# Performance work log

Hardware: AMD Instinct MI355X
Metric: run time of the kernel (lower is better)

Reference implementation:

```python
import jax, jax.numpy as jnp
import numpy as np

B, A, H, V, L = 8192, 128, 256, 64, 20


def setup_inputs() -> dict:
    key = jax.random.key(0)
    ks = jax.random.split(key, 9)
    s = lambda k, sh: jax.random.normal(k, sh, dtype=jnp.float32) * 0.05
    return {
        "attrVector": jax.random.normal(ks[0], (B, A), dtype=jnp.float32),
        "W_a": s(ks[1], (H, A)), "b_a": s(ks[2], (H,)),
        "W_ih": s(ks[3], (4 * H, V)), "W_hh": s(ks[4], (4 * H, H)),
        "b_ih": s(ks[5], (4 * H,)), "b_hh": s(ks[6], (4 * H,)),
        "W_v": s(ks[7], (V, H)), "b_v": s(ks[8], (V,)),
    }


def _lstm_step(x, h, c, W_ih, W_hh, b_ih, b_hh):
    # PyTorch LSTM gate order: input, forget, cell(g), output
    gates = x @ W_ih.T + b_ih + h @ W_hh.T + b_hh  # [B, 4H]
    i, f, g, o = jnp.split(gates, 4, axis=-1)
    c_new = jax.nn.sigmoid(f) * c + jax.nn.sigmoid(i) * jnp.tanh(g)
    h_new = jax.nn.sigmoid(o) * jnp.tanh(c_new)
    return h_new, c_new


def reference(attrVector, W_a, b_a, W_ih, W_hh, b_ih, b_hh, W_v, b_v):
    batch = attrVector.shape[0]
    dt = attrVector.dtype
    # attr2hidden -> initial hidden state; cell state zeros (init_hidden)
    h = attrVector @ W_a.T + b_a                      # [B, H]
    c = jnp.zeros_like(h)
    # start-token step (all-zeros embedding)
    x0 = jnp.zeros((batch, V), dtype=dt)
    h, c = _lstm_step(x0, h, c, W_ih, W_hh, b_ih, b_hh)

    keys = jax.random.split(jax.random.key(42), L)

    def step(carry, k):
        h, c, slp, plp, ep = carry
        logits = h @ W_v.T + b_v                      # [B, V]
        logp = jax.nn.log_softmax(logits, axis=-1)
        plp = plp + jnp.sum(jnp.exp(logp) * logp, axis=-1)  # negative entropy
        ch = jax.random.categorical(k, logits, axis=-1)     # [B] int sample
        lp = jnp.take_along_axis(logp, ch[:, None], axis=-1)[:, 0]
        slp = slp + lp
        ep = ep * jnp.exp(lp)
        x = jax.nn.one_hot(ch, V, dtype=dt)
        h2, c2 = _lstm_step(x, h, c, W_ih, W_hh, b_ih, b_hh)
        return (h2, c2, slp, plp, ep), ch

    zeros = jnp.zeros((batch,), dtype=dt)
    ones = jnp.ones((batch,), dtype=dt)
    (_, _, slp, plp, ep), msgs = jax.lax.scan(step, (h, c, zeros, zeros, ones), keys)
    message = msgs.T.astype(jnp.int64) if msgs.dtype != jnp.int64 else msgs.T  # [B, L]
    return message, slp, plp, ep
```

## Files before the change

### kernel.cpp

```cpp
#include <hip/hip_runtime.h>
#include <stdint.h>

#define BATCH 8192
#define ADIM 128
#define HDIM 256
#define VDIM 64
#define NSTEP 20
#define TB 16
#define HSP 20

typedef union { float4 v; float f[4]; } F4;

__device__ __forceinline__ uint32_t rotl32(uint32_t x, uint32_t d) {
  return (x << d) | (x >> (32u - d));
}
__device__ __forceinline__ void tf4(uint32_t& x0, uint32_t& x1, int r0, int r1, int r2, int r3) {
  x0 += x1; x1 = rotl32(x1, r0); x1 ^= x0;
  x0 += x1; x1 = rotl32(x1, r1); x1 ^= x0;
  x0 += x1; x1 = rotl32(x1, r2); x1 ^= x0;
  x0 += x1; x1 = rotl32(x1, r3); x1 ^= x0;
}
__device__ __forceinline__ void threefry2x32(uint32_t k0, uint32_t k1, uint32_t x0, uint32_t x1,
                                             uint32_t& o0, uint32_t& o1) {
  uint32_t k2 = k0 ^ k1 ^ 0x1BD11BDAu;
  x0 += k0; x1 += k1;
  tf4(x0, x1, 13, 15, 26, 6);  x0 += k1; x1 += k2 + 1u;
  tf4(x0, x1, 17, 29, 16, 24); x0 += k2; x1 += k0 + 2u;
  tf4(x0, x1, 13, 15, 26, 6);  x0 += k0; x1 += k1 + 3u;
  tf4(x0, x1, 17, 29, 16, 24); x0 += k1; x1 += k2 + 4u;
  tf4(x0, x1, 13, 15, 26, 6);  x0 += k2; x1 += k0 + 5u;
  o0 = x0; o1 = x1;
}

__device__ __forceinline__ float sigm(float x) { return 1.0f / (1.0f + expf(-x)); }

__global__ void prep_kernel(const float* __restrict__ Whh, const float* __restrict__ Wv,
                            const float* __restrict__ Wa, const float* __restrict__ Wih,
                            float* __restrict__ ws) {
  int n = blockIdx.x * blockDim.x + threadIdx.x;
  int stride = gridDim.x * blockDim.x;
  float* WhhT4 = ws;
  float* WvT   = ws + 262144;
  float* WaT   = ws + 278528;
  float* WihT4 = ws + 311296;
  for (int i = n; i < 256 * 1024; i += stride) {
    int k = i >> 10, rem = i & 1023, u = rem >> 2, g = rem & 3;
    WhhT4[i] = Whh[((g << 8) + u) * 256 + k];
  }
  for (int i = n; i < 256 * 64; i += stride) { int k = i >> 6, v = i & 63; WvT[i] = Wv[v * 256 + k]; }
  for (int i = n; i < 128 * 256; i += stride) { int k = i >> 8, u = i & 255; WaT[i] = Wa[u * 128 + k]; }
  for (int i = n; i < 64 * 1024; i += stride) {
    int v = i >> 10, rem = i & 1023, u = rem >> 2, g = rem & 3;
    WihT4[i] = Wih[((g << 8) + u) * 64 + v];
  }
}

__global__ __launch_bounds__(256, 2) void sender_main(
    const float* __restrict__ attr, const float* __restrict__ b_a,
    const float* __restrict__ b_ih, const float* __restrict__ b_hh,
    const float* __restrict__ b_v,
    const float* __restrict__ WhhT4, const float* __restrict__ WvT,
    const float* __restrict__ WaT, const float* __restrict__ WihT4,
    float* __restrict__ out) {
  __shared__ float h_s[HDIM][HSP];
  __shared__ float attr_s[ADIM][HSP];
  __shared__ float slp_s[TB], plp_s[TB], ep_s[TB];
  __shared__ int ch_s[TB];

  const int tid = threadIdx.x;
  const int w = tid >> 6;
  const int lane = tid & 63;
  const int u = (w << 6) + lane;
  const int w4 = w << 2;
  const int b0 = blockIdx.x * TB;

  if (tid < TB) { slp_s[tid] = 0.0f; plp_s[tid] = 0.0f; ep_s[tid] = 1.0f; }

  {
    int r = tid >> 5;
    int cm = (tid & 31) << 2;
    #pragma unroll
    for (int pass = 0; pass < 2; ++pass) {
      int row = r + (pass << 3);
      F4 vv; vv.v = *(const float4*)&attr[(size_t)(b0 + row) * ADIM + cm];
      attr_s[cm + 0][row] = vv.f[0];
      attr_s[cm + 1][row] = vv.f[1];
      attr_s[cm + 2][row] = vv.f[2];
      attr_s[cm + 3][row] = vv.f[3];
    }
  }
  __syncthreads();

  {
    float acc[16];
    #pragma unroll
    for (int s = 0; s < 16; ++s) acc[s] = 0.0f;
    #pragma unroll 2
    for (int k = 0; k < ADIM; ++k) {
      F4 a0, a1, a2, a3;
      a0.v = *(const float4*)&attr_s[k][0];
      a1.v = *(const float4*)&attr_s[k][4];
      a2.v = *(const float4*)&attr_s[k][8];
      a3.v = *(const float4*)&attr_s[k][12];
      float wa = WaT[(k << 8) + u];
      #pragma unroll
      for (int j = 0; j < 4; ++j) {
        acc[j]      = fmaf(a0.f[j], wa, acc[j]);
        acc[4 + j]  = fmaf(a1.f[j], wa, acc[4 + j]);
        acc[8 + j]  = fmaf(a2.f[j], wa, acc[8 + j]);
        acc[12 + j] = fmaf(a3.f[j], wa, acc[12 + j]);
      }
    }
    float ba = b_a[u];
    #pragma unroll
    for (int q = 0; q < 4; ++q) {
      F4 hv4;
      #pragma unroll
      for (int j = 0; j < 4; ++j) hv4.f[j] = acc[q * 4 + j] + ba;
      *(float4*)&h_s[u][q * 4] = hv4.v;
    }
  }
  __syncthreads();

  float c_r[16];
  #pragma unroll
  for (int s = 0; s < 16; ++s) c_r[s] = 0.0f;

  float bg[4];
  #pragma unroll
  for (int g = 0; g < 4; ++g) bg[g] = b_ih[(g << 8) + u] + b_hh[(g << 8) + u];
  const float bv = b_v[lane];

  {
    float ga[16][4];
    #pragma unroll
    for (int s = 0; s < 16; ++s)
      #pragma unroll
      for (int g = 0; g < 4; ++g) ga[s][g] = 0.0f;
    #pragma unroll 2
    for (int k = 0; k < HDIM; ++k) {
      F4 h0q, h1q, h2q, h3q;
      h0q.v = *(const float4*)&h_s[k][0];
      h1q.v = *(const float4*)&h_s[k][4];
      h2q.v = *(const float4*)&h_s[k][8];
      h3q.v = *(const float4*)&h_s[k][12];
      F4 wv4; wv4.v = *(const float4*)&WhhT4[(k << 10) + (u << 2)];
      #pragma unroll
      for (int j = 0; j < 4; ++j) {
        #pragma unroll
        for (int g = 0; g < 4; ++g) {
          ga[j][g]      = fmaf(h0q.f[j], wv4.f[g], ga[j][g]);
          ga[4 + j][g]  = fmaf(h1q.f[j], wv4.f[g], ga[4 + j][g]);
          ga[8 + j][g]  = fmaf(h2q.f[j], wv4.f[g], ga[8 + j][g]);
          ga[12 + j][g] = fmaf(h3q.f[j], wv4.f[g], ga[12 + j][g]);
        }
      }
    }
    __syncthreads();
    float hn[16];
    #pragma unroll
    for (int s = 0; s < 16; ++s) {
      float gi = ga[s][0] + bg[0];
      float gf = ga[s][1] + bg[1];
      float gg = ga[s][2] + bg[2];
      float go = ga[s][3] + bg[3];
      float cn = sigm(gf) * c_r[s] + sigm(gi) * tanhf(gg);
      hn[s] = sigm(go) * tanhf(cn);
      c_r[s] = cn;
    }
    #pragma unroll
    for (int q = 0; q < 4; ++q) {
      F4 hv4;
      #pragma unroll
      for (int j = 0; j < 4; ++j) hv4.f[j] = hn[q * 4 + j];
      *(float4*)&h_s[u][q * 4] = hv4.v;
    }
    __syncthreads();
  }

  for (int l = 0; l < NSTEP; ++l) {
    uint32_t kl0, kl1;
    threefry2x32(0u, 42u, 0u, (uint32_t)l, kl0, kl1);

    const bool last = (l == NSTEP - 1);
    float la[4] = {0.0f, 0.0f, 0.0f, 0.0f};
    float ga[16][4];
    #pragma unroll
    for (int s = 0; s < 16; ++s)
      #pragma unroll
      for (int g = 0; g < 4; ++g) ga[s][g] = 0.0f;

    if (!last) {
      #pragma unroll 2
      for (int k = 0; k < HDIM; ++k) {
        F4 h0q, h1q, h2q, h3q, hl;
        h0q.v = *(const float4*)&h_s[k][0];
        h1q.v = *(const float4*)&h_s[k][4];
        h2q.v = *(const float4*)&h_s[k][8];
        h3q.v = *(const float4*)&h_s[k][12];
        hl.v  = *(const float4*)&h_s[k][w4];
        F4 wv4; wv4.v = *(const float4*)&WhhT4[(k << 10) + (u << 2)];
        float wvv = WvT[(k << 6) | lane];
        #pragma unroll
        for (int s = 0; s < 4; ++s) la[s] = fmaf(hl.f[s], wvv, la[s]);
        #pragma unroll
        for (int j = 0; j < 4; ++j) {
          #pragma unroll
          for (int g = 0; g < 4; ++g) {
            ga[j][g]      = fmaf(h0q.f[j], wv4.f[g], ga[j][g]);
            ga[4 + j][g]  = fmaf(h1q.f[j], wv4.f[g], ga[4 + j][g]);
            ga[8 + j][g]  = fmaf(h2q.f[j], wv4.f[g], ga[8 + j][g]);
            ga[12 + j][g] = fmaf(h3q.f[j], wv4.f[g], ga[12 + j][g]);
          }
        }
      }
    } else {
      #pragma unroll 2
      for (int k = 0; k < HDIM; ++k) {
        F4 hl; hl.v = *(const float4*)&h_s[k][w4];
        float wvv = WvT[(k << 6) | lane];
        #pragma unroll
        for (int s = 0; s < 4; ++s) la[s] = fmaf(hl.f[s], wvv, la[s]);
      }
    }

    #pragma unroll
    for (int db = 0; db < 4; ++db) {
      float x = la[db] + bv;
      float m = x;
      #pragma unroll
      for (int o = 32; o > 0; o >>= 1) m = fmaxf(m, __shfl_xor(m, o));
      float e = expf(x - m);
      float s = e;
      #pragma unroll
      for (int o = 32; o > 0; o >>= 1) s += __shfl_xor(s, o);
      float lse = logf(s);
      float logp = x - m - lse;
      float p = expf(logp);
      float pe = p * logp;
      #pragma unroll
      for (int o = 32; o > 0; o >>= 1) pe += __shfl_xor(pe, o);
      uint32_t idx = ((uint32_t)(b0 + w4 + db) << 6) | (uint32_t)lane;
      uint32_t r0, r1;
      threefry2x32(kl0, kl1, 0u, idx, r0, r1);
      uint32_t bits = r0 ^ r1;
      float f01 = __uint_as_float((bits >> 9) | 0x3f800000u) - 1.0f;
      const float TINY = 1.17549435e-38f;
      float uu2 = fmaxf(TINY, f01 + TINY);
      float gn = -logf(-logf(uu2));
      float y = gn + x;
      float by = y; int bi = lane;
      #pragma unroll
      for (int o = 32; o > 0; o >>= 1) {
        float oy = __shfl_xor(by, o);
        int oi = __shfl_xor(bi, o);
        if (oy > by || (oy == by && oi < bi)) { by = oy; bi = oi; }
      }
      float lp = __shfl(logp, bi, 64);
      if (lane == 0) {
        int bb = w4 + db;
        ch_s[bb] = bi;
        slp_s[bb] += lp;
        plp_s[bb] += pe;
        ep_s[bb] *= expf(lp);
        out[(size_t)(b0 + bb) * NSTEP + l] = (float)bi;
      }
    }

    if (!last) {
      __syncthreads();
      float hn[16];
      #pragma unroll
      for (int s = 0; s < 16; ++s) {
        F4 wi; wi.v = *(const float4*)&WihT4[(ch_s[s] << 10) + (u << 2)];
        float gi = ga[s][0] + wi.f[0] + bg[0];
        float gf = ga[s][1] + wi.f[1] + bg[1];
        float gg = ga[s][2] + wi.f[2] + bg[2];
        float go = ga[s][3] + wi.f[3] + bg[3];
        float cn = sigm(gf) * c_r[s] + sigm(gi) * tanhf(gg);
        hn[s] = sigm(go) * tanhf(cn);
        c_r[s] = cn;
      }
      #pragma unroll
      for (int q = 0; q < 4; ++q) {
        F4 hv4;
        #pragma unroll
        for (int j = 0; j < 4; ++j) hv4.f[j] = hn[q * 4 + j];
        *(float4*)&h_s[u][q * 4] = hv4.v;
      }
      __syncthreads();
    }
  }

  __syncthreads();
  if (tid < TB) {
    int bb = b0 + tid;
    out[(size_t)BATCH * NSTEP + bb]             = slp_s[tid];
    out[(size_t)BATCH * NSTEP + BATCH + bb]     = plp_s[tid];
    out[(size_t)BATCH * NSTEP + 2 * BATCH + bb] = ep_s[tid];
  }
}

extern "C" void kernel_launch(void* const* d_in, const int* in_sizes, int n_in,
                              void* d_out, int out_size, void* d_ws, size_t ws_size,
                              hipStream_t stream) {
  const float* attr = (const float*)d_in[0];
  const float* W_a  = (const float*)d_in[1];
  const float* b_a  = (const float*)d_in[2];
  const float* W_ih = (const float*)d_in[3];
  const float* W_hh = (const float*)d_in[4];
  const float* b_ih = (const float*)d_in[5];
  const float* b_hh = (const float*)d_in[6];
  const float* W_v  = (const float*)d_in[7];
  const float* b_v  = (const float*)d_in[8];
  float* ws = (float*)d_ws;

  prep_kernel<<<256, 256, 0, stream>>>(W_hh, W_v, W_a, W_ih, ws);
  sender_main<<<BATCH / TB, 256, 0, stream>>>(
      attr, b_a, b_ih, b_hh, b_v,
      ws, ws + 262144, ws + 278528, ws + 311296,
      (float*)d_out);
}
```

Measured before the change: 1.525 ms.

## Broadcast hidden state via readlane instead of LDS float4 reads in recurrent matvec

Replaces the per-k shared-memory float4 broadcasts of the hidden state with a per-chunk load of 16 k-values into registers, followed by v_readlane broadcasts inside the FMA loop. This is meant to cut LDS traffic and LDS-issue pressure in the dominant W_hh matvec. Batch slots are rotated per wave by w4 so each wave's own four samples sit in slots 0-3 for the fused logits. The h_s padding changes to 17 with scalar stores to avoid bank conflicts. The cost is many readlane instructions (SALU/VALU interplay) and higher register pressure from holding the 16-entry hch chunk.

```diff
diff --git a/kernel.cpp b/kernel.cpp
--- a/kernel.cpp
+++ b/kernel.cpp
@@ -7,7 +7,8 @@
 #define VDIM 64
 #define NSTEP 20
 #define TB 16
-#define HSP 20
+#define HSP 17
+#define ASP 20
 
 typedef union { float4 v; float f[4]; } F4;
 
@@ -33,6 +34,10 @@
 }
 
 __device__ __forceinline__ float sigm(float x) { return 1.0f / (1.0f + expf(-x)); }
+
+__device__ __forceinline__ float bcast(float x, int t) {
+  return __int_as_float(__builtin_amdgcn_readlane(__float_as_int(x), t));
+}
 
 __global__ void prep_kernel(const float* __restrict__ Whh, const float* __restrict__ Wv,
                             const float* __restrict__ Wa, const float* __restrict__ Wih,
@@ -63,7 +68,7 @@
     const float* __restrict__ WaT, const float* __restrict__ WihT4,
     float* __restrict__ out) {
   __shared__ float h_s[HDIM][HSP];
-  __shared__ float attr_s[ADIM][HSP];
+  __shared__ __align__(16) float attr_s[ADIM][ASP];
   __shared__ float slp_s[TB], plp_s[TB], ep_s[TB];
   __shared__ int ch_s[TB];
 
@@ -113,12 +118,7 @@
     }
     float ba = b_a[u];
     #pragma unroll
-    for (int q = 0; q < 4; ++q) {
-      F4 hv4;
-      #pragma unroll
-      for (int j = 0; j < 4; ++j) hv4.f[j] = acc[q * 4 + j] + ba;
-      *(float4*)&h_s[u][q * 4] = hv4.v;
-    }
+    for (int s = 0; s < 16; ++s) h_s[u][s] = acc[s] + ba;
   }
   __syncthreads();
 
@@ -137,22 +137,24 @@
     for (int s = 0; s < 16; ++s)
       #pragma unroll
       for (int g = 0; g < 4; ++g) ga[s][g] = 0.0f;
-    #pragma unroll 2
-    for (int k = 0; k < HDIM; ++k) {
-      F4 h0q, h1q, h2q, h3q;
-      h0q.v = *(const float4*)&h_s[k][0];
-      h1q.v = *(const float4*)&h_s[k][4];
-      h2q.v = *(const float4*)&h_s[k][8];
-      h3q.v = *(const float4*)&h_s[k][12];
-      F4 wv4; wv4.v = *(const float4*)&WhhT4[(k << 10) + (u << 2)];
-      #pragma unroll
-      for (int j = 0; j < 4; ++j) {
-        #pragma unroll
-        for (int g = 0; g < 4; ++g) {
-          ga[j][g]      = fmaf(h0q.f[j], wv4.f[g], ga[j][g]);
-          ga[4 + j][g]  = fmaf(h1q.f[j], wv4.f[g], ga[4 + j][g]);
-          ga[8 + j][g]  = fmaf(h2q.f[j], wv4.f[g], ga[8 + j][g]);
-          ga[12 + j][g] = fmaf(h3q.f[j], wv4.f[g], ga[12 + j][g]);
+    #pragma unroll 1
+    for (int kc = 0; kc < 16; ++kc) {
+      const int k0 = kc << 4;
+      const int kk = k0 + (lane & 15);
+      float hch[16];
+      #pragma unroll
+      for (int s = 0; s < 16; ++s) hch[s] = h_s[kk][(s + w4) & 15];
+      #pragma unroll
+      for (int t = 0; t < 16; ++t) {
+        const int k = k0 + t;
+        F4 wv4; wv4.v = *(const float4*)&WhhT4[(k << 10) + (u << 2)];
+        #pragma unroll
+        for (int s = 0; s < 16; ++s) {
+          float hb = bcast(hch[s], t);
+          ga[s][0] = fmaf(hb, wv4.f[0], ga[s][0]);
+          ga[s][1] = fmaf(hb, wv4.f[1], ga[s][1]);
+          ga[s][2] = fmaf(hb, wv4.f[2], ga[s][2]);
+          ga[s][3] = fmaf(hb, wv4.f[3], ga[s][3]);
         }
       }
     }
@@ -169,15 +171,11 @@
       c_r[s] = cn;
     }
     #pragma unroll
-    for (int q = 0; q < 4; ++q) {
-      F4 hv4;
-      #pragma unroll
-      for (int j = 0; j < 4; ++j) hv4.f[j] = hn[q * 4 + j];
-      *(float4*)&h_s[u][q * 4] = hv4.v;
-    }
+    for (int s = 0; s < 16; ++s) h_s[u][(s + w4) & 15] = hn[s];
     __syncthreads();
   }
 
+  #pragma unroll 1
   for (int l = 0; l < NSTEP; ++l) {
     uint32_t kl0, kl1;
     threefry2x32(0u, 42u, 0u, (uint32_t)l, kl0, kl1);
@@ -191,36 +189,44 @@
       for (int g = 0; g < 4; ++g) ga[s][g] = 0.0f;
 
     if (!last) {
-      #pragma unroll 2
-      for (int k = 0; k < HDIM; ++k) {
-        F4 h0q, h1q, h2q, h3q, hl;
-        h0q.v = *(const float4*)&h_s[k][0];
-        h1q.v = *(const float4*)&h_s[k][4];
-        h2q.v = *(const float4*)&h_s[k][8];
-        h3q.v = *(const float4*)&h_s[k][12];
-        hl.v  = *(const float4*)&h_s[k][w4];
-        F4 wv4; wv4.v = *(const float4*)&WhhT4[(k << 10) + (u << 2)];
-        float wvv = WvT[(k << 6) | lane];
-        #pragma unroll
-        for (int s = 0; s < 4; ++s) la[s] = fmaf(hl.f[s], wvv, la[s]);
-        #pragma unroll
-        for (int j = 0; j < 4; ++j) {
+      #pragma unroll 1
+      for (int kc = 0; kc < 16; ++kc) {
+        const int k0 = kc << 4;
+        const int kk = k0 + (lane & 15);
+        float hch[16];
+        #pragma unroll
+        for (int s = 0; s < 16; ++s) hch[s] = h_s[kk][(s + w4) & 15];
+        #pragma unroll
+        for (int t = 0; t < 16; ++t) {
+          const int k = k0 + t;
+          F4 wv4; wv4.v = *(const float4*)&WhhT4[(k << 10) + (u << 2)];
+          float wvv = WvT[(k << 6) | lane];
           #pragma unroll
-          for (int g = 0; g < 4; ++g) {
-            ga[j][g]      = fmaf(h0q.f[j], wv4.f[g], ga[j][g]);
-            ga[4 + j][g]  = fmaf(h1q.f[j], wv4.f[g], ga[4 + j][g]);
-            ga[8 + j][g]  = fmaf(h2q.f[j], wv4.f[g], ga[8 + j][g]);
-            ga[12 + j][g] = fmaf(h3q.f[j], wv4.f[g], ga[12 + j][g]);
+          for (int s = 0; s < 16; ++s) {
+            float hb = bcast(hch[s], t);
+            if (s < 4) la[s] = fmaf(hb, wvv, la[s]);
+            ga[s][0] = fmaf(hb, wv4.f[0], ga[s][0]);
+            ga[s][1] = fmaf(hb, wv4.f[1], ga[s][1]);
+            ga[s][2] = fmaf(hb, wv4.f[2], ga[s][2]);
+            ga[s][3] = fmaf(hb, wv4.f[3], ga[s][3]);
           }
         }
       }
     } else {
-      #pragma unroll 2
-      for (int k = 0; k < HDIM; ++k) {
-        F4 hl; hl.v = *(const float4*)&h_s[k][w4];
-        float wvv = WvT[(k << 6) | lane];
-        #pragma unroll
-        for (int s = 0; s < 4; ++s) la[s] = fmaf(hl.f[s], wvv, la[s]);
+      #pragma unroll 1
+      for (int kc = 0; kc < 16; ++kc) {
+        const int k0 = kc << 4;
+        const int kk = k0 + (lane & 15);
+        float hch[4];
+        #pragma unroll
+        for (int s = 0; s < 4; ++s) hch[s] = h_s[kk][(s + w4) & 15];
+        #pragma unroll
+        for (int t = 0; t < 16; ++t) {
+          const int k = k0 + t;
+          float wvv = WvT[(k << 6) | lane];
+          #pragma unroll
+          for (int s = 0; s < 4; ++s) la[s] = fmaf(bcast(hch[s], t), wvv, la[s]);
+        }
       }
     }
 
@@ -272,7 +278,8 @@
       float hn[16];
       #pragma unroll
       for (int s = 0; s < 16; ++s) {
-        F4 wi; wi.v = *(const float4*)&WihT4[(ch_s[s] << 10) + (u << 2)];
+        const int sp = (s + w4) & 15;
+        F4 wi; wi.v = *(const float4*)&WihT4[(ch_s[sp] << 10) + (u << 2)];
         float gi = ga[s][0] + wi.f[0] + bg[0];
         float gf = ga[s][1] + wi.f[1] + bg[1];
         float gg = ga[s][2] + wi.f[2] + bg[2];
@@ -282,12 +289,7 @@
         c_r[s] = cn;
       }
       #pragma unroll
-      for (int q = 0; q < 4; ++q) {
-        F4 hv4;
-        #pragma unroll
-        for (int j = 0; j < 4; ++j) hv4.f[j] = hn[q * 4 + j];
-        *(float4*)&h_s[u][q * 4] = hv4.v;
-      }
+      for (int s = 0; s < 16; ++s) h_s[u][(s + w4) & 15] = hn[s];
       __syncthreads();
     }
   }
```

Measured after the change: 1.441 ms. 5.5% less time.
